# Performance work log

Measured on AMD Instinct MI355X. Metric: run time of the kernel, lower is better.

## Reference

```python
import jax, jax.numpy as jnp
import numpy as np

B, H, S, D = 4, 16, 2048, 64

def setup_inputs() -> dict:
    key = jax.random.key(0)
    kq, kk, kv = jax.random.split(key, 3)
    Q = jax.random.normal(kq, (B, H, S, D), dtype=jnp.float32)
    K = jax.random.normal(kk, (B, H, S, D), dtype=jnp.float32)
    V = jax.random.normal(kv, (B, H, S, D), dtype=jnp.float32)
    return {"Q": Q, "K": K, "V": V}

def reference(Q, K, V):
    d_model = Q.shape[-1]
    # [B,H,S,S] scores matrix, materialized as in the original (unfused SDPA)
    scores = jnp.einsum('bhqd,bhkd->bhqk', Q, K) / jnp.sqrt(jnp.float32(d_model))
    attention = jax.nn.softmax(scores, axis=-1)
    out = jnp.einsum('bhqk,bhkd->bhqd', attention, V)
    return out
```

## Files before the change

kernel.cpp:

```cpp
#include <hip/hip_runtime.h>
#include <hip/hip_bf16.h>

namespace {

constexpr int kSeq = 2048;
constexpr int kD   = 64;
constexpr int kBH  = 64;
constexpr int kQB  = 256;
constexpr int kBN  = 64;
constexpr int kNT  = kSeq / kBN;
constexpr int kGrid = kBH * (kSeq / kQB);
constexpr int kPs  = 72;

typedef __attribute__((ext_vector_type(8))) short bf16x8;
typedef __attribute__((ext_vector_type(4))) float f32x4;
typedef __attribute__((ext_vector_type(2))) unsigned int u32x2;
typedef __attribute__((ext_vector_type(4))) unsigned int u32x4;

__device__ __forceinline__ unsigned short f2bf(float f) {
  unsigned int u = __builtin_bit_cast(unsigned int, f);
  u += 0x7fffu + ((u >> 16) & 1u);
  return (unsigned short)(u >> 16);
}

__device__ __forceinline__ unsigned int pkbf(float a, float b) {
#if __has_builtin(__builtin_amdgcn_cvt_pk_bf16_f32)
  typedef __attribute__((ext_vector_type(2))) __bf16 bfv2;
  bfv2 r = __builtin_amdgcn_cvt_pk_bf16_f32(a, b);
  return __builtin_bit_cast(unsigned int, r);
#else
  unsigned int ua = __builtin_bit_cast(unsigned int, a) + 0x8000u;
  unsigned int ub = __builtin_bit_cast(unsigned int, b) + 0x8000u;
  return __builtin_amdgcn_perm(ub, ua, 0x07060302);
#endif
}

__device__ __forceinline__ float fexp2(float x) {
#if __has_builtin(__builtin_amdgcn_exp2f)
  return __builtin_amdgcn_exp2f(x);
#else
  return exp2f(x);
#endif
}

__device__ __forceinline__ u32x2 plswap32(unsigned int a, unsigned int b) {
#if __has_builtin(__builtin_amdgcn_permlane32_swap)
  return __builtin_amdgcn_permlane32_swap(a, b, false, false);
#else
  const int lane = threadIdx.x & 63;
  unsigned int sa = __shfl_xor(a, 32, 64), sb = __shfl_xor(b, 32, 64);
  u32x2 r;
  r[0] = (lane < 32) ? a : sb;
  r[1] = (lane < 32) ? sa : b;
  return r;
#endif
}

__device__ __forceinline__ u32x2 plswap16(unsigned int a, unsigned int b) {
#if __has_builtin(__builtin_amdgcn_permlane16_swap)
  return __builtin_amdgcn_permlane16_swap(a, b, false, false);
#else
  const int lane = threadIdx.x & 63;
  unsigned int sa = __shfl_xor(a, 16, 64), sb = __shfl_xor(b, 16, 64);
  const bool even = ((lane >> 4) & 1) == 0;
  u32x2 r;
  r[0] = even ? a : sb;
  r[1] = even ? sa : b;
  return r;
#endif
}

__device__ __forceinline__ void load16(const unsigned short* g, unsigned short* l) {
  __builtin_amdgcn_global_load_lds(
      (const __attribute__((address_space(1))) unsigned int*)g,
      (__attribute__((address_space(3))) unsigned int*)l, 16, 0, 0);
}

__global__ __launch_bounds__(256) void prep(
    const float* __restrict__ K, const float* __restrict__ V,
    unsigned short* __restrict__ Kbf, unsigned short* __restrict__ Vt) {
  __shared__ float sTf[kD * 65];
  const int tid = threadIdx.x;
  const int bh = blockIdx.x >> 5;
  const int t0 = (blockIdx.x & 31) * 64;
  const float* Kb = K + ((size_t)bh * kSeq + t0) * kD;
  const float* Vb = V + ((size_t)bh * kSeq + t0) * kD;
  unsigned short* Ko = Kbf + ((size_t)bh * kSeq + t0) * kD;
#pragma unroll
  for (int t = 0; t < 4; ++t) {
    const int idx = tid + t * 256;
    const int row = idx >> 4;
    const int c4  = (idx & 15) * 4;
    const float4 k4 = *(const float4*)(Kb + row * kD + c4);
    u32x2 kp = {pkbf(k4.x, k4.y), pkbf(k4.z, k4.w)};
    *(u32x2*)(Ko + row * kD + c4) = kp;
    const float4 v4 = *(const float4*)(Vb + row * kD + c4);
    sTf[(c4 + 0) * 65 + row] = v4.x;
    sTf[(c4 + 1) * 65 + row] = v4.y;
    sTf[(c4 + 2) * 65 + row] = v4.z;
    sTf[(c4 + 3) * 65 + row] = v4.w;
  }
  __syncthreads();
  const int d = tid >> 2, q = tid & 3;
  const float* ts = &sTf[d * 65 + q * 16];
  float p[16];
#pragma unroll
  for (int j = 0; j < 16; ++j) p[j] = ts[j];
  uint4 a, b;
  a.x = pkbf(p[0], p[1]);   a.y = pkbf(p[2], p[3]);
  a.z = pkbf(p[4], p[5]);   a.w = pkbf(p[6], p[7]);
  b.x = pkbf(p[8], p[9]);   b.y = pkbf(p[10], p[11]);
  b.z = pkbf(p[12], p[13]); b.w = pkbf(p[14], p[15]);
  unsigned short* vo = Vt + ((size_t)bh * kD + d) * kSeq + t0 + q * 16;
  *(uint4*)(vo)     = a;
  *(uint4*)(vo + 8) = b;
}

__global__ __launch_bounds__(512, 4) void fattn8r(
    const float* __restrict__ Q, const unsigned short* __restrict__ Kbf,
    const unsigned short* __restrict__ Vt, float* __restrict__ O) {
  __shared__ unsigned short sK[2][kBN * kD];
  __shared__ unsigned short sV[2][kD * kBN];

  const int tid  = threadIdx.x;
  const int wave = tid >> 6;
  const int lane = tid & 63;
  const int quad = lane >> 4;
  const int l16  = lane & 15;
  const int swz  = l16 & 7;

  const int x  = blockIdx.x & 7;
  const int j  = blockIdx.x >> 3;
  const int bh = x * 8 + (j >> 3);
  const int q0 = (j & 7) * kQB;
  const size_t kb = (size_t)bh * kSeq * kD;

  constexpr float cs = 0.18033688011112042f;

  bf16x8 qf[2][2];
#pragma unroll
  for (int mt = 0; mt < 2; ++mt) {
    const float* qr =
        Q + kb + (size_t)(q0 + wave * 32 + mt * 16 + l16) * kD + quad * 8;
#pragma unroll
    for (int kc = 0; kc < 2; ++kc)
#pragma unroll
      for (int jj = 0; jj < 8; ++jj)
        qf[mt][kc][jj] = (short)f2bf(qr[kc * 32 + jj] * cs);
  }

  bf16x8 ones;
#pragma unroll
  for (int jj = 0; jj < 8; ++jj) ones[jj] = (short)0x3F80;

  const int r0 = tid >> 3, c0 = (tid & 7) ^ (r0 & 7);
  const unsigned short* kg0 = Kbf + kb + r0 * kD + c0 * 8;
  const unsigned short* vg0 = Vt + kb + r0 * kSeq + c0 * 8;

  f32x4 o[2][4];
#pragma unroll
  for (int mt = 0; mt < 2; ++mt)
#pragma unroll
    for (int dt = 0; dt < 4; ++dt) o[mt][dt] = (f32x4){0.f, 0.f, 0.f, 0.f};
  f32x4 lacc[2] = {(f32x4){0.f, 0.f, 0.f, 0.f}, (f32x4){0.f, 0.f, 0.f, 0.f}};

  load16(kg0, &sK[0][tid * 8]);
  load16(vg0, &sV[0][tid * 8]);

  for (int t = 0; t < kNT; ++t) {
    const int p = t & 1;
    __syncthreads();
    if (t + 1 < kNT) {
      const int pn = p ^ 1;
      const size_t ko = (size_t)(t + 1) * kBN * kD;
      const int vo = (t + 1) * kBN;
      load16(kg0 + ko, &sK[pn][tid * 8]);
      load16(vg0 + vo, &sV[pn][tid * 8]);
    }
    const unsigned short* sKp = sK[p];
    const unsigned short* sVp = sV[p];

    f32x4 sA[4], sB[4];
#pragma unroll
    for (int nt = 0; nt < 4; ++nt) {
      sA[nt] = (f32x4){0.f, 0.f, 0.f, 0.f};
      sB[nt] = (f32x4){0.f, 0.f, 0.f, 0.f};
    }
    __builtin_amdgcn_s_setprio(1);
#pragma unroll
    for (int kc = 0; kc < 2; ++kc)
#pragma unroll
      for (int nt = 0; nt < 4; ++nt) {
        const bf16x8 kf = *(const bf16x8*)&sKp[(nt * 16 + l16) * kD +
                                              (((kc * 4 + quad) ^ swz) * 8)];
        sA[nt] = __builtin_amdgcn_mfma_f32_16x16x32_bf16(kf, qf[0][kc], sA[nt], 0, 0, 0);
        sB[nt] = __builtin_amdgcn_mfma_f32_16x16x32_bf16(kf, qf[1][kc], sB[nt], 0, 0, 0);
      }
    __builtin_amdgcn_s_setprio(0);

    bf16x8 afA[2], afB[2];
#pragma unroll
    for (int kc = 0; kc < 2; ++kc) {
      u32x2 xa0 = {pkbf(fexp2(sA[2 * kc][0]), fexp2(sA[2 * kc][1])),
                   pkbf(fexp2(sA[2 * kc][2]), fexp2(sA[2 * kc][3]))};
      u32x2 xa1 = {pkbf(fexp2(sA[2 * kc + 1][0]), fexp2(sA[2 * kc + 1][1])),
                   pkbf(fexp2(sA[2 * kc + 1][2]), fexp2(sA[2 * kc + 1][3]))};
      u32x2 wa0 = plswap32(xa0[0], xa1[0]);
      u32x2 za0 = plswap16(wa0[0], wa0[1]);
      u32x2 wa1 = plswap32(xa0[1], xa1[1]);
      u32x2 za1 = plswap16(wa1[0], wa1[1]);
      u32x4 av = {za0[0], za1[0], za0[1], za1[1]};
      afA[kc] = __builtin_bit_cast(bf16x8, av);

      u32x2 xb0 = {pkbf(fexp2(sB[2 * kc][0]), fexp2(sB[2 * kc][1])),
                   pkbf(fexp2(sB[2 * kc][2]), fexp2(sB[2 * kc][3]))};
      u32x2 xb1 = {pkbf(fexp2(sB[2 * kc + 1][0]), fexp2(sB[2 * kc + 1][1])),
                   pkbf(fexp2(sB[2 * kc + 1][2]), fexp2(sB[2 * kc + 1][3]))};
      u32x2 wb0 = plswap32(xb0[0], xb1[0]);
      u32x2 zb0 = plswap16(wb0[0], wb0[1]);
      u32x2 wb1 = plswap32(xb0[1], xb1[1]);
      u32x2 zb1 = plswap16(wb1[0], wb1[1]);
      u32x4 bv = {zb0[0], zb1[0], zb0[1], zb1[1]};
      afB[kc] = __builtin_bit_cast(bf16x8, bv);
    }

    __builtin_amdgcn_s_setprio(1);
#pragma unroll
    for (int kc = 0; kc < 2; ++kc) {
      const int ac = ((kc * 4 + quad) ^ swz) * 8;
      lacc[0] = __builtin_amdgcn_mfma_f32_16x16x32_bf16(afA[kc], ones, lacc[0], 0, 0, 0);
      lacc[1] = __builtin_amdgcn_mfma_f32_16x16x32_bf16(afB[kc], ones, lacc[1], 0, 0, 0);
#pragma unroll
      for (int dt = 0; dt < 4; ++dt) {
        const bf16x8 vf = *(const bf16x8*)&sVp[(dt * 16 + l16) * kBN + ac];
        o[0][dt] = __builtin_amdgcn_mfma_f32_16x16x32_bf16(afA[kc], vf, o[0][dt], 0, 0, 0);
        o[1][dt] = __builtin_amdgcn_mfma_f32_16x16x32_bf16(afB[kc], vf, o[1][dt], 0, 0, 0);
      }
    }
    __builtin_amdgcn_s_setprio(0);
  }

#pragma unroll
  for (int mt = 0; mt < 2; ++mt) {
    float* Ob = O + kb + (size_t)(q0 + wave * 32 + mt * 16) * kD;
#pragma unroll
    for (int r = 0; r < 4; ++r) {
      const float inv = 1.f / lacc[mt][r];
#pragma unroll
      for (int dt = 0; dt < 4; ++dt)
        Ob[(quad * 4 + r) * kD + dt * 16 + l16] = o[mt][dt][r] * inv;
    }
  }
}

__global__ __launch_bounds__(256, 4) void fattn_fb(
    const float* __restrict__ Q, const float* __restrict__ K,
    const float* __restrict__ V, float* __restrict__ O) {
  __shared__ unsigned short sK[kBN * kPs];
  __shared__ unsigned short sV[kD * kPs];
  __shared__ unsigned short sP[4 * 16 * kPs];
  const int tid = threadIdx.x, wave = tid >> 6, lane = tid & 63;
  const int quad = lane >> 4, l16 = lane & 15;
  const int bh = blockIdx.x >> 5, q0 = (blockIdx.x & 31) * 64;
  const float* Qb = Q + (size_t)bh * kSeq * kD;
  const float* Kb = K + (size_t)bh * kSeq * kD;
  const float* Vb = V + (size_t)bh * kSeq * kD;
  bf16x8 qf[2];
  {
    const float* qr = Qb + (size_t)(q0 + wave * 16 + l16) * kD + quad * 8;
#pragma unroll
    for (int kc = 0; kc < 2; ++kc)
#pragma unroll
      for (int jj = 0; jj < 8; ++jj) qf[kc][jj] = (short)f2bf(qr[kc * 32 + jj]);
  }
  f32x4 o[4];
#pragma unroll
  for (int dt = 0; dt < 4; ++dt) o[dt] = (f32x4){0.f, 0.f, 0.f, 0.f};
  float lsum[4] = {0.f, 0.f, 0.f, 0.f};
  constexpr float cs = 0.18033688011112042f;
  unsigned short* pw = &sP[wave * 16 * kPs];
  for (int kv0 = 0; kv0 < kSeq; kv0 += kBN) {
    __syncthreads();
#pragma unroll
    for (int t = 0; t < 4; ++t) {
      const int idx = tid + t * 256;
      const int row = idx >> 4, c4 = (idx & 15) * 4;
      const float4 k4 = *(const float4*)(Kb + (size_t)(kv0 + row) * kD + c4);
      unsigned short* kd = &sK[row * kPs + c4];
      kd[0] = f2bf(k4.x); kd[1] = f2bf(k4.y); kd[2] = f2bf(k4.z); kd[3] = f2bf(k4.w);
      const float4 v4 = *(const float4*)(Vb + (size_t)(kv0 + row) * kD + c4);
      sV[(c4 + 0) * kPs + row] = f2bf(v4.x);
      sV[(c4 + 1) * kPs + row] = f2bf(v4.y);
      sV[(c4 + 2) * kPs + row] = f2bf(v4.z);
      sV[(c4 + 3) * kPs + row] = f2bf(v4.w);
    }
    __syncthreads();
    f32x4 s[4];
#pragma unroll
    for (int nt = 0; nt < 4; ++nt) s[nt] = (f32x4){0.f, 0.f, 0.f, 0.f};
#pragma unroll
    for (int kc = 0; kc < 2; ++kc)
#pragma unroll
      for (int nt = 0; nt < 4; ++nt) {
        const bf16x8 kf = *(const bf16x8*)&sK[(nt * 16 + l16) * kPs + kc * 32 + quad * 8];
        s[nt] = __builtin_amdgcn_mfma_f32_16x16x32_bf16(qf[kc], kf, s[nt], 0, 0, 0);
      }
#pragma unroll
    for (int nt = 0; nt < 4; ++nt)
#pragma unroll
      for (int r = 0; r < 4; ++r) {
        const float p = fexp2(s[nt][r] * cs);
        lsum[r] += p;
        pw[(quad * 4 + r) * kPs + nt * 16 + l16] = f2bf(p);
      }
#pragma unroll
    for (int kc = 0; kc < 2; ++kc) {
      const bf16x8 af = *(const bf16x8*)&pw[l16 * kPs + kc * 32 + quad * 8];
#pragma unroll
      for (int dt = 0; dt < 4; ++dt) {
        const bf16x8 vf = *(const bf16x8*)&sV[(dt * 16 + l16) * kPs + kc * 32 + quad * 8];
        o[dt] = __builtin_amdgcn_mfma_f32_16x16x32_bf16(af, vf, o[dt], 0, 0, 0);
      }
    }
  }
#pragma unroll
  for (int r = 0; r < 4; ++r)
#pragma unroll
    for (int off = 1; off < 16; off <<= 1)
      lsum[r] += __shfl_xor(lsum[r], off, 64);
  float* Ob = O + (size_t)bh * kSeq * kD + (size_t)(q0 + wave * 16) * kD;
#pragma unroll
  for (int r = 0; r < 4; ++r) {
    const float inv = 1.f / lsum[r];
#pragma unroll
    for (int dt = 0; dt < 4; ++dt)
      Ob[(quad * 4 + r) * kD + dt * 16 + l16] = o[dt][r] * inv;
  }
}

}

extern "C" void kernel_launch(void* const* d_in, const int* in_sizes, int n_in,
                              void* d_out, int out_size, void* d_ws, size_t ws_size,
                              hipStream_t stream) {
  const float* Q = (const float*)d_in[0];
  const float* K = (const float*)d_in[1];
  const float* V = (const float*)d_in[2];
  float* Oo = (float*)d_out;
  const size_t need = (size_t)2 * kBH * kSeq * kD * sizeof(unsigned short);
  if (ws_size >= need) {
    unsigned short* Kbf = (unsigned short*)d_ws;
    unsigned short* Vt  = Kbf + (size_t)kBH * kSeq * kD;
    prep<<<dim3(kBH * (kSeq / 64)), dim3(256), 0, stream>>>(K, V, Kbf, Vt);
    fattn8r<<<dim3(kGrid), dim3(512), 0, stream>>>(Q, Kbf, Vt, Oo);
  } else {
    fattn_fb<<<dim3(kBH * (kSeq / 64)), dim3(256), 0, stream>>>(Q, K, V, Oo);
  }
}
```

Before: 201.6 us.

## Fuse K/V bf16 conversion and V transpose into the attention kernel

Removes the separate prep kernel that converted K and V to bf16 (and transposed V) through a workspace. The attention kernel now streams fp32 K/V tiles into LDS with direct global-to-LDS loads, converts and transposes them in-kernel into swizzled bf16 double buffers, and overlaps this with the QK MFMAs. This drops one launch and the workspace round trip. In exchange each block of the 8 that share a head redoes the conversion, global traffic for K/V doubles because fp32 is read, and LDS use grows with 32 KB of fp32 staging. The fallback kernel is also removed.

```diff
diff --git a/kernel.cpp b/kernel.cpp
--- a/kernel.cpp
+++ b/kernel.cpp
@@ -10,7 +10,6 @@
 constexpr int kBN  = 64;
 constexpr int kNT  = kSeq / kBN;
 constexpr int kGrid = kBH * (kSeq / kQB);
-constexpr int kPs  = 72;
 
 typedef __attribute__((ext_vector_type(8))) short bf16x8;
 typedef __attribute__((ext_vector_type(4))) float f32x4;
@@ -70,57 +69,19 @@
 #endif
 }
 
-__device__ __forceinline__ void load16(const unsigned short* g, unsigned short* l) {
+__device__ __forceinline__ void load16f(const float* g, unsigned short* l) {
   __builtin_amdgcn_global_load_lds(
       (const __attribute__((address_space(1))) unsigned int*)g,
       (__attribute__((address_space(3))) unsigned int*)l, 16, 0, 0);
 }
 
-__global__ __launch_bounds__(256) void prep(
-    const float* __restrict__ K, const float* __restrict__ V,
-    unsigned short* __restrict__ Kbf, unsigned short* __restrict__ Vt) {
-  __shared__ float sTf[kD * 65];
-  const int tid = threadIdx.x;
-  const int bh = blockIdx.x >> 5;
-  const int t0 = (blockIdx.x & 31) * 64;
-  const float* Kb = K + ((size_t)bh * kSeq + t0) * kD;
-  const float* Vb = V + ((size_t)bh * kSeq + t0) * kD;
-  unsigned short* Ko = Kbf + ((size_t)bh * kSeq + t0) * kD;
-#pragma unroll
-  for (int t = 0; t < 4; ++t) {
-    const int idx = tid + t * 256;
-    const int row = idx >> 4;
-    const int c4  = (idx & 15) * 4;
-    const float4 k4 = *(const float4*)(Kb + row * kD + c4);
-    u32x2 kp = {pkbf(k4.x, k4.y), pkbf(k4.z, k4.w)};
-    *(u32x2*)(Ko + row * kD + c4) = kp;
-    const float4 v4 = *(const float4*)(Vb + row * kD + c4);
-    sTf[(c4 + 0) * 65 + row] = v4.x;
-    sTf[(c4 + 1) * 65 + row] = v4.y;
-    sTf[(c4 + 2) * 65 + row] = v4.z;
-    sTf[(c4 + 3) * 65 + row] = v4.w;
-  }
-  __syncthreads();
-  const int d = tid >> 2, q = tid & 3;
-  const float* ts = &sTf[d * 65 + q * 16];
-  float p[16];
-#pragma unroll
-  for (int j = 0; j < 16; ++j) p[j] = ts[j];
-  uint4 a, b;
-  a.x = pkbf(p[0], p[1]);   a.y = pkbf(p[2], p[3]);
-  a.z = pkbf(p[4], p[5]);   a.w = pkbf(p[6], p[7]);
-  b.x = pkbf(p[8], p[9]);   b.y = pkbf(p[10], p[11]);
-  b.z = pkbf(p[12], p[13]); b.w = pkbf(p[14], p[15]);
-  unsigned short* vo = Vt + ((size_t)bh * kD + d) * kSeq + t0 + q * 16;
-  *(uint4*)(vo)     = a;
-  *(uint4*)(vo + 8) = b;
-}
-
-__global__ __launch_bounds__(512, 4) void fattn8r(
-    const float* __restrict__ Q, const unsigned short* __restrict__ Kbf,
-    const unsigned short* __restrict__ Vt, float* __restrict__ O) {
+__global__ __launch_bounds__(512, 4) void fattn_c(
+    const float* __restrict__ Q, const float* __restrict__ K,
+    const float* __restrict__ V, float* __restrict__ O) {
   __shared__ unsigned short sK[2][kBN * kD];
   __shared__ unsigned short sV[2][kD * kBN];
+  __shared__ float sFK[kBN * kD];
+  __shared__ float sFV[kBN * kD];
 
   const int tid  = threadIdx.x;
   const int wave = tid >> 6;
@@ -152,10 +113,14 @@
   bf16x8 ones;
 #pragma unroll
   for (int jj = 0; jj < 8; ++jj) ones[jj] = (short)0x3F80;
-
-  const int r0 = tid >> 3, c0 = (tid & 7) ^ (r0 & 7);
-  const unsigned short* kg0 = Kbf + kb + r0 * kD + c0 * 8;
-  const unsigned short* vg0 = Vt + kb + r0 * kSeq + c0 * 8;
+  const f32x4 zc = (f32x4){0.f, 0.f, 0.f, 0.f};
+
+  const float* kgA = K + kb + (size_t)(tid >> 4) * kD + (tid & 15) * 4;
+  const float* vgA = V + kb + (size_t)(tid >> 4) * kD + (tid & 15) * 4;
+  unsigned short* fk1 = (unsigned short*)sFK + tid * 8;
+  unsigned short* fk2 = (unsigned short*)sFK + (tid + 512) * 8;
+  unsigned short* fv1 = (unsigned short*)sFV + tid * 8;
+  unsigned short* fv2 = (unsigned short*)sFV + (tid + 512) * 8;
 
   f32x4 o[2][4];
 #pragma unroll
@@ -164,39 +129,78 @@
     for (int dt = 0; dt < 4; ++dt) o[mt][dt] = (f32x4){0.f, 0.f, 0.f, 0.f};
   f32x4 lacc[2] = {(f32x4){0.f, 0.f, 0.f, 0.f}, (f32x4){0.f, 0.f, 0.f, 0.f}};
 
-  load16(kg0, &sK[0][tid * 8]);
-  load16(vg0, &sV[0][tid * 8]);
+  auto stage = [&](int tt) {
+    const size_t off = (size_t)tt * (kBN * kD);
+    load16f(kgA + off, fk1);
+    load16f(kgA + off + 32 * kD, fk2);
+    load16f(vgA + off, fv1);
+    load16f(vgA + off + 32 * kD, fv2);
+  };
+  auto convert = [&](int pn) {
+    const float4 ka = *(const float4*)&sFK[tid * 4];
+    const float4 kb4 = *(const float4*)&sFK[(tid + 512) * 4];
+    u32x2 ua = {pkbf(ka.x, ka.y), pkbf(ka.z, ka.w)};
+    u32x2 ub = {pkbf(kb4.x, kb4.y), pkbf(kb4.z, kb4.w)};
+    const int r1 = tid >> 4;
+    const int cK = (tid & 15) >> 1;
+    const int h4 = (tid & 1) << 2;
+    *(u32x2*)&sK[pn][r1 * 64 + ((cK ^ (r1 & 7)) << 3) + h4] = ua;
+    const int r2 = r1 + 32;
+    *(u32x2*)&sK[pn][r2 * 64 + ((cK ^ (r2 & 7)) << 3) + h4] = ub;
+    const int rA = 4 * wave;
+    const float v0 = sFV[(rA + 0) * 64 + lane];
+    const float v1 = sFV[(rA + 1) * 64 + lane];
+    const float v2 = sFV[(rA + 2) * 64 + lane];
+    const float v3 = sFV[(rA + 3) * 64 + lane];
+    const float w0 = sFV[(rA + 32) * 64 + lane];
+    const float w1 = sFV[(rA + 33) * 64 + lane];
+    const float w2 = sFV[(rA + 34) * 64 + lane];
+    const float w3 = sFV[(rA + 35) * 64 + lane];
+    u32x2 pa = {pkbf(v0, v1), pkbf(v2, v3)};
+    u32x2 pb = {pkbf(w0, w1), pkbf(w2, w3)};
+    const int sd = lane & 7;
+    const int cv = wave >> 1;
+    const int hv4 = (wave & 1) << 2;
+    *(u32x2*)&sV[pn][lane * 64 + ((cv ^ sd) << 3) + hv4] = pa;
+    *(u32x2*)&sV[pn][lane * 64 + (((cv + 4) ^ sd) << 3) + hv4] = pb;
+  };
+
+  stage(0);
+  asm volatile("s_waitcnt vmcnt(0)" ::: "memory");
+  __builtin_amdgcn_sched_barrier(0);
+  convert(0);
+  asm volatile("s_waitcnt lgkmcnt(0)" ::: "memory");
+  __builtin_amdgcn_sched_barrier(0);
+  stage(1);
 
   for (int t = 0; t < kNT; ++t) {
     const int p = t & 1;
     __syncthreads();
+
+    f32x4 sA[4], sB[4];
+    __builtin_amdgcn_s_setprio(1);
+#pragma unroll
+    for (int nt = 0; nt < 4; ++nt) {
+      const bf16x8 kf = *(const bf16x8*)&sK[p][(nt * 16 + l16) * kD +
+                                             ((quad ^ swz) * 8)];
+      sA[nt] = __builtin_amdgcn_mfma_f32_16x16x32_bf16(kf, qf[0][0], zc, 0, 0, 0);
+      sB[nt] = __builtin_amdgcn_mfma_f32_16x16x32_bf16(kf, qf[1][0], zc, 0, 0, 0);
+    }
+#pragma unroll
+    for (int nt = 0; nt < 4; ++nt) {
+      const bf16x8 kf = *(const bf16x8*)&sK[p][(nt * 16 + l16) * kD +
+                                             (((4 + quad) ^ swz) * 8)];
+      sA[nt] = __builtin_amdgcn_mfma_f32_16x16x32_bf16(kf, qf[0][1], sA[nt], 0, 0, 0);
+      sB[nt] = __builtin_amdgcn_mfma_f32_16x16x32_bf16(kf, qf[1][1], sB[nt], 0, 0, 0);
+    }
+    __builtin_amdgcn_s_setprio(0);
+
     if (t + 1 < kNT) {
-      const int pn = p ^ 1;
-      const size_t ko = (size_t)(t + 1) * kBN * kD;
-      const int vo = (t + 1) * kBN;
-      load16(kg0 + ko, &sK[pn][tid * 8]);
-      load16(vg0 + vo, &sV[pn][tid * 8]);
-    }
-    const unsigned short* sKp = sK[p];
-    const unsigned short* sVp = sV[p];
-
-    f32x4 sA[4], sB[4];
-#pragma unroll
-    for (int nt = 0; nt < 4; ++nt) {
-      sA[nt] = (f32x4){0.f, 0.f, 0.f, 0.f};
-      sB[nt] = (f32x4){0.f, 0.f, 0.f, 0.f};
-    }
-    __builtin_amdgcn_s_setprio(1);
-#pragma unroll
-    for (int kc = 0; kc < 2; ++kc)
-#pragma unroll
-      for (int nt = 0; nt < 4; ++nt) {
-        const bf16x8 kf = *(const bf16x8*)&sKp[(nt * 16 + l16) * kD +
-                                              (((kc * 4 + quad) ^ swz) * 8)];
-        sA[nt] = __builtin_amdgcn_mfma_f32_16x16x32_bf16(kf, qf[0][kc], sA[nt], 0, 0, 0);
-        sB[nt] = __builtin_amdgcn_mfma_f32_16x16x32_bf16(kf, qf[1][kc], sB[nt], 0, 0, 0);
-      }
-    __builtin_amdgcn_s_setprio(0);
+      convert(p ^ 1);
+      asm volatile("s_waitcnt lgkmcnt(0)" ::: "memory");
+      __builtin_amdgcn_sched_barrier(0);
+      if (t + 2 < kNT) stage(t + 2);
+    }
 
     bf16x8 afA[2], afB[2];
 #pragma unroll
@@ -232,7 +236,7 @@
       lacc[1] = __builtin_amdgcn_mfma_f32_16x16x32_bf16(afB[kc], ones, lacc[1], 0, 0, 0);
 #pragma unroll
       for (int dt = 0; dt < 4; ++dt) {
-        const bf16x8 vf = *(const bf16x8*)&sVp[(dt * 16 + l16) * kBN + ac];
+        const bf16x8 vf = *(const bf16x8*)&sV[p][(dt * 16 + l16) * kBN + ac];
         o[0][dt] = __builtin_amdgcn_mfma_f32_16x16x32_bf16(afA[kc], vf, o[0][dt], 0, 0, 0);
         o[1][dt] = __builtin_amdgcn_mfma_f32_16x16x32_bf16(afB[kc], vf, o[1][dt], 0, 0, 0);
       }
@@ -250,91 +254,6 @@
       for (int dt = 0; dt < 4; ++dt)
         Ob[(quad * 4 + r) * kD + dt * 16 + l16] = o[mt][dt][r] * inv;
     }
-  }
-}
-
-__global__ __launch_bounds__(256, 4) void fattn_fb(
-    const float* __restrict__ Q, const float* __restrict__ K,
-    const float* __restrict__ V, float* __restrict__ O) {
-  __shared__ unsigned short sK[kBN * kPs];
-  __shared__ unsigned short sV[kD * kPs];
-  __shared__ unsigned short sP[4 * 16 * kPs];
-  const int tid = threadIdx.x, wave = tid >> 6, lane = tid & 63;
-  const int quad = lane >> 4, l16 = lane & 15;
-  const int bh = blockIdx.x >> 5, q0 = (blockIdx.x & 31) * 64;
-  const float* Qb = Q + (size_t)bh * kSeq * kD;
-  const float* Kb = K + (size_t)bh * kSeq * kD;
-  const float* Vb = V + (size_t)bh * kSeq * kD;
-  bf16x8 qf[2];
-  {
-    const float* qr = Qb + (size_t)(q0 + wave * 16 + l16) * kD + quad * 8;
-#pragma unroll
-    for (int kc = 0; kc < 2; ++kc)
-#pragma unroll
-      for (int jj = 0; jj < 8; ++jj) qf[kc][jj] = (short)f2bf(qr[kc * 32 + jj]);
-  }
-  f32x4 o[4];
-#pragma unroll
-  for (int dt = 0; dt < 4; ++dt) o[dt] = (f32x4){0.f, 0.f, 0.f, 0.f};
-  float lsum[4] = {0.f, 0.f, 0.f, 0.f};
-  constexpr float cs = 0.18033688011112042f;
-  unsigned short* pw = &sP[wave * 16 * kPs];
-  for (int kv0 = 0; kv0 < kSeq; kv0 += kBN) {
-    __syncthreads();
-#pragma unroll
-    for (int t = 0; t < 4; ++t) {
-      const int idx = tid + t * 256;
-      const int row = idx >> 4, c4 = (idx & 15) * 4;
-      const float4 k4 = *(const float4*)(Kb + (size_t)(kv0 + row) * kD + c4);
-      unsigned short* kd = &sK[row * kPs + c4];
-      kd[0] = f2bf(k4.x); kd[1] = f2bf(k4.y); kd[2] = f2bf(k4.z); kd[3] = f2bf(k4.w);
-      const float4 v4 = *(const float4*)(Vb + (size_t)(kv0 + row) * kD + c4);
-      sV[(c4 + 0) * kPs + row] = f2bf(v4.x);
-      sV[(c4 + 1) * kPs + row] = f2bf(v4.y);
-      sV[(c4 + 2) * kPs + row] = f2bf(v4.z);
-      sV[(c4 + 3) * kPs + row] = f2bf(v4.w);
-    }
-    __syncthreads();
-    f32x4 s[4];
-#pragma unroll
-    for (int nt = 0; nt < 4; ++nt) s[nt] = (f32x4){0.f, 0.f, 0.f, 0.f};
-#pragma unroll
-    for (int kc = 0; kc < 2; ++kc)
-#pragma unroll
-      for (int nt = 0; nt < 4; ++nt) {
-        const bf16x8 kf = *(const bf16x8*)&sK[(nt * 16 + l16) * kPs + kc * 32 + quad * 8];
-        s[nt] = __builtin_amdgcn_mfma_f32_16x16x32_bf16(qf[kc], kf, s[nt], 0, 0, 0);
-      }
-#pragma unroll
-    for (int nt = 0; nt < 4; ++nt)
-#pragma unroll
-      for (int r = 0; r < 4; ++r) {
-        const float p = fexp2(s[nt][r] * cs);
-        lsum[r] += p;
-        pw[(quad * 4 + r) * kPs + nt * 16 + l16] = f2bf(p);
-      }
-#pragma unroll
-    for (int kc = 0; kc < 2; ++kc) {
-      const bf16x8 af = *(const bf16x8*)&pw[l16 * kPs + kc * 32 + quad * 8];
-#pragma unroll
-      for (int dt = 0; dt < 4; ++dt) {
-        const bf16x8 vf = *(const bf16x8*)&sV[(dt * 16 + l16) * kPs + kc * 32 + quad * 8];
-        o[dt] = __builtin_amdgcn_mfma_f32_16x16x32_bf16(af, vf, o[dt], 0, 0, 0);
-      }
-    }
-  }
-#pragma unroll
-  for (int r = 0; r < 4; ++r)
-#pragma unroll
-    for (int off = 1; off < 16; off <<= 1)
-      lsum[r] += __shfl_xor(lsum[r], off, 64);
-  float* Ob = O + (size_t)bh * kSeq * kD + (size_t)(q0 + wave * 16) * kD;
-#pragma unroll
-  for (int r = 0; r < 4; ++r) {
-    const float inv = 1.f / lsum[r];
-#pragma unroll
-    for (int dt = 0; dt < 4; ++dt)
-      Ob[(quad * 4 + r) * kD + dt * 16 + l16] = o[dt][r] * inv;
   }
 }
 
@@ -347,13 +266,6 @@
   const float* K = (const float*)d_in[1];
   const float* V = (const float*)d_in[2];
   float* Oo = (float*)d_out;
-  const size_t need = (size_t)2 * kBH * kSeq * kD * sizeof(unsigned short);
-  if (ws_size >= need) {
-    unsigned short* Kbf = (unsigned short*)d_ws;
-    unsigned short* Vt  = Kbf + (size_t)kBH * kSeq * kD;
-    prep<<<dim3(kBH * (kSeq / 64)), dim3(256), 0, stream>>>(K, V, Kbf, Vt);
-    fattn8r<<<dim3(kGrid), dim3(512), 0, stream>>>(Q, Kbf, Vt, Oo);
-  } else {
-    fattn_fb<<<dim3(kBH * (kSeq / 64)), dim3(256), 0, stream>>>(Q, K, V, Oo);
-  }
-}
+  (void)d_ws; (void)ws_size;
+  fattn_c<<<dim3(kGrid), dim3(512), 0, stream>>>(Q, K, V, Oo);
+}
```

Result: faster. 192.5 us, median of 2 (-4.5%).
